# Kernel tuning notes

Hardware: AMD Instinct MI355X
Metric: run time of the kernel (lower is better)

Reference implementation:

```python
import jax, jax.numpy as jnp
import numpy as np
from jax import lax

T_STEPS = 4
TAU = 2.0
V_THRESHOLD = 1.0
V_RESET = 0.0
ATAN_ALPHA = 2.0

@jax.custom_vjp
def atan_spike(x):
    # Heaviside forward, ATan surrogate gradient (spikingjelly surrogate.ATan, alpha=2)
    return (x >= 0.0).astype(x.dtype)

def _atan_fwd(x):
    return atan_spike(x), x

def _atan_bwd(x, g):
    grad = (ATAN_ALPHA / 2.0) / (1.0 + (jnp.pi / 2.0 * ATAN_ALPHA * x) ** 2)
    return (g * grad,)

atan_spike.defvjp(_atan_fwd, _atan_bwd)

def setup_inputs() -> dict:
    key = jax.random.key(0)
    inputs = jax.random.normal(key, (32, 720, 862), dtype=jnp.float32)  # B, L, C
    return {"inputs": inputs}

def reference(inputs) -> jnp.ndarray:
    # repeat along a new leading time dim: (T, B, L, C)
    x = jnp.broadcast_to(inputs[None], (T_STEPS,) + inputs.shape)
    # permute(0,1,3,2) -> (T, B, C, L)
    x = jnp.transpose(x, (0, 1, 3, 2))

    def step(v, xt):
        # LIF with decay_input=True (spikingjelly default):
        # v <- v + (x - (v - v_reset)) / tau
        v = v + (xt - (v - V_RESET)) / TAU
        s = atan_spike(v - V_THRESHOLD)
        sd = lax.stop_gradient(s)  # detach_reset=True
        v = (1.0 - sd) * v + sd * V_RESET  # hard reset
        return v, s

    v0 = jnp.zeros_like(x[0])
    _, spks = lax.scan(step, v0, x)
    return spks  # (T, B, C, L)
```

## Files before the change

### kernel.cpp

```cpp
#include <hip/hip_runtime.h>


#define B_DIM 32
#define L_DIM 720
#define C_DIM 862
#define T_STEPS 4
#define TL 64
#define TC 64
#define LROW 68

typedef float v2f __attribute__((ext_vector_type(2)));
typedef float v4f __attribute__((ext_vector_type(4)));

__global__ __launch_bounds__(256)
void lif_repeat_encoder(const float* __restrict__ in, float* __restrict__ out) {
    __shared__ float smem[TC * LROW];

    const int b   = blockIdx.z;
    const int l0  = blockIdx.x * TL;
    const int c0  = blockIdx.y * TC;
    const int tid = threadIdx.x;

    const float* __restrict__ inb = in + (size_t)b * (L_DIM * C_DIM);

    {
        const int c4   = (tid & 15) << 2;
        const int lrow = tid >> 4;
#pragma unroll
        for (int p = 0; p < 4; ++p) {
            const int ll = lrow + p * 16;
            const int l  = l0 + ll;
            if (l < L_DIM) {
                const int c = c0 + c4;
                const float* src = inb + (size_t)l * C_DIM + c;
                if (c + 3 < C_DIM) {
                    const v2f a = *(const v2f*)(src);
                    const v2f d = *(const v2f*)(src + 2);
                    smem[(c4 + 0) * LROW + ll] = a.x;
                    smem[(c4 + 1) * LROW + ll] = a.y;
                    smem[(c4 + 2) * LROW + ll] = d.x;
                    smem[(c4 + 3) * LROW + ll] = d.y;
                } else {
#pragma unroll
                    for (int i = 0; i < 4; ++i) {
                        if (c + i < C_DIM)
                            smem[(c4 + i) * LROW + ll] = src[i];
                    }
                }
            }
        }
    }
    __syncthreads();

    const int l4   = (tid & 15) << 2;
    const int crow = tid >> 4;
    const int l    = l0 + l4;
    if (l >= L_DIM) return;

    const size_t plane = (size_t)B_DIM * C_DIM * L_DIM;

#pragma unroll
    for (int q = 0; q < 4; ++q) {
        const int cl = crow + q * 16;
        const int c  = c0 + cl;
        if (c >= C_DIM) continue;

        const v4f x = *(const v4f*)(smem + cl * LROW + l4);

        float sx[T_STEPS], sy[T_STEPS], sz[T_STEPS], sw[T_STEPS];
        {
            float v0 = 0.f, v1 = 0.f, v2 = 0.f, v3 = 0.f;
#pragma unroll
            for (int t = 0; t < T_STEPS; ++t) {
                v0 += (x.x - v0) * 0.5f;
                v1 += (x.y - v1) * 0.5f;
                v2 += (x.z - v2) * 0.5f;
                v3 += (x.w - v3) * 0.5f;
                sx[t] = (v0 >= 1.0f) ? 1.0f : 0.0f;
                sy[t] = (v1 >= 1.0f) ? 1.0f : 0.0f;
                sz[t] = (v2 >= 1.0f) ? 1.0f : 0.0f;
                sw[t] = (v3 >= 1.0f) ? 1.0f : 0.0f;
                v0 = (v0 >= 1.0f) ? 0.0f : v0;
                v1 = (v1 >= 1.0f) ? 0.0f : v1;
                v2 = (v2 >= 1.0f) ? 0.0f : v2;
                v3 = (v3 >= 1.0f) ? 0.0f : v3;
            }
        }

        const size_t base = ((size_t)b * C_DIM + c) * L_DIM + l;
#pragma unroll
        for (int t = 0; t < T_STEPS; ++t) {
            v4f o;
            o.x = sx[t]; o.y = sy[t]; o.z = sz[t]; o.w = sw[t];
            __builtin_nontemporal_store(o, (v4f*)(out + (size_t)t * plane + base));
        }
    }
}

extern "C" void kernel_launch(void* const* d_in, const int* in_sizes, int n_in,
                              void* d_out, int out_size, void* d_ws, size_t ws_size,
                              hipStream_t stream) {
    const float* in = (const float*)d_in[0];
    float* out = (float*)d_out;

    dim3 block(256, 1, 1);
    dim3 grid((L_DIM + TL - 1) / TL,
              (C_DIM + TC - 1) / TC,
              B_DIM);

    lif_repeat_encoder<<<grid, block, 0, stream>>>(in, out);
}
```

Measured before the change: 379.4 us.

## Retile transpose to full-L column strips of 16 channels per block

Each block now loads all 720 rows for a 16-channel strip into shared memory and writes whole contiguous output rows of L. Each wave handles 4 channels and sweeps the full L dimension, so the stores cover full rows instead of 64-element fragments. The intent is better write coalescing and fewer partial tiles along L. The cost is narrower input reads (8-byte loads across 16 channels, 64 bytes per row) and more shared memory per block (about 46KB), which lowers occupancy.

```diff
diff --git a/kernel.cpp b/kernel.cpp
--- a/kernel.cpp
+++ b/kernel.cpp
@@ -5,46 +5,41 @@
 #define L_DIM 720
 #define C_DIM 862
 #define T_STEPS 4
-#define TL 64
-#define TC 64
-#define LROW 68
+#define TC 16
+#define SL 724
 
 typedef float v2f __attribute__((ext_vector_type(2)));
 typedef float v4f __attribute__((ext_vector_type(4)));
 
 __global__ __launch_bounds__(256)
 void lif_repeat_encoder(const float* __restrict__ in, float* __restrict__ out) {
-    __shared__ float smem[TC * LROW];
+    __shared__ float sm[TC * SL];
 
-    const int b   = blockIdx.z;
-    const int l0  = blockIdx.x * TL;
-    const int c0  = blockIdx.y * TC;
+    const int b   = blockIdx.y;
+    const int c0  = blockIdx.x * TC;
     const int tid = threadIdx.x;
 
     const float* __restrict__ inb = in + (size_t)b * (L_DIM * C_DIM);
 
     {
-        const int c4   = (tid & 15) << 2;
-        const int lrow = tid >> 4;
+        const int cl2 = (tid & 7) << 1;
+        const int c   = c0 + cl2;
+        const int r0  = tid >> 3;
+        if (c < C_DIM) {
+            for (int base = 0; base < L_DIM; base += 128) {
+                v2f v[4];
 #pragma unroll
-        for (int p = 0; p < 4; ++p) {
-            const int ll = lrow + p * 16;
-            const int l  = l0 + ll;
-            if (l < L_DIM) {
-                const int c = c0 + c4;
-                const float* src = inb + (size_t)l * C_DIM + c;
-                if (c + 3 < C_DIM) {
-                    const v2f a = *(const v2f*)(src);
-                    const v2f d = *(const v2f*)(src + 2);
-                    smem[(c4 + 0) * LROW + ll] = a.x;
-                    smem[(c4 + 1) * LROW + ll] = a.y;
-                    smem[(c4 + 2) * LROW + ll] = d.x;
-                    smem[(c4 + 3) * LROW + ll] = d.y;
-                } else {
+                for (int u = 0; u < 4; ++u) {
+                    const int r = base + r0 + 32 * u;
+                    if (r < L_DIM)
+                        v[u] = *(const v2f*)(inb + (size_t)r * C_DIM + c);
+                }
 #pragma unroll
-                    for (int i = 0; i < 4; ++i) {
-                        if (c + i < C_DIM)
-                            smem[(c4 + i) * LROW + ll] = src[i];
+                for (int u = 0; u < 4; ++u) {
+                    const int r = base + r0 + 32 * u;
+                    if (r < L_DIM) {
+                        sm[cl2 * SL + r]       = v[u].x;
+                        sm[(cl2 + 1) * SL + r] = v[u].y;
                     }
                 }
             }
@@ -52,23 +47,26 @@
     }
     __syncthreads();
 
-    const int l4   = (tid & 15) << 2;
-    const int crow = tid >> 4;
-    const int l    = l0 + l4;
-    if (l >= L_DIM) return;
-
+    const int wave = tid >> 6;
+    const int lane = tid & 63;
     const size_t plane = (size_t)B_DIM * C_DIM * L_DIM;
 
 #pragma unroll
     for (int q = 0; q < 4; ++q) {
-        const int cl = crow + q * 16;
+        const int cl = wave * 4 + q;
         const int c  = c0 + cl;
         if (c >= C_DIM) continue;
 
-        const v4f x = *(const v4f*)(smem + cl * LROW + l4);
+        const size_t rowbase = ((size_t)b * C_DIM + c) * L_DIM;
 
-        float sx[T_STEPS], sy[T_STEPS], sz[T_STEPS], sw[T_STEPS];
-        {
+#pragma unroll
+        for (int round = 0; round < 3; ++round) {
+            const int j = lane + 64 * round;
+            if (j >= L_DIM / 4) break;
+
+            const v4f x = *(const v4f*)(sm + cl * SL + 4 * j);
+
+            float sx[T_STEPS], sy[T_STEPS], sz[T_STEPS], sw[T_STEPS];
             float v0 = 0.f, v1 = 0.f, v2 = 0.f, v3 = 0.f;
 #pragma unroll
             for (int t = 0; t < T_STEPS; ++t) {
@@ -85,14 +83,14 @@
                 v2 = (v2 >= 1.0f) ? 0.0f : v2;
                 v3 = (v3 >= 1.0f) ? 0.0f : v3;
             }
-        }
 
-        const size_t base = ((size_t)b * C_DIM + c) * L_DIM + l;
 #pragma unroll
-        for (int t = 0; t < T_STEPS; ++t) {
-            v4f o;
-            o.x = sx[t]; o.y = sy[t]; o.z = sz[t]; o.w = sw[t];
-            __builtin_nontemporal_store(o, (v4f*)(out + (size_t)t * plane + base));
+            for (int t = 0; t < T_STEPS; ++t) {
+                v4f o;
+                o.x = sx[t]; o.y = sy[t]; o.z = sz[t]; o.w = sw[t];
+                __builtin_nontemporal_store(
+                    o, (v4f*)(out + (size_t)t * plane + rowbase + 4 * j));
+            }
         }
     }
 }
@@ -104,9 +102,9 @@
     float* out = (float*)d_out;
 
     dim3 block(256, 1, 1);
-    dim3 grid((L_DIM + TL - 1) / TL,
-              (C_DIM + TC - 1) / TC,
-              B_DIM);
+    dim3 grid((C_DIM + TC - 1) / TC,
+              B_DIM,
+              1);
 
     lif_repeat_encoder<<<grid, block, 0, stream>>>(in, out);
 }
```

Result: faster. 369.2 us (-2.7%).
